# Kernel optimization log

Measured on AMD Instinct MI355X. Metric: run time of the kernel, lower is better.

## Reference

```python
import jax, jax.numpy as jnp
import numpy as np

NPOINT, K = 1024, 16
BN_EPS = 1e-5


def farthest_point_sample(xyz, npoint):
    # xyz: [B, N, 3]. Deterministic start at index 0 (torch version uses randint).
    B, N, _ = xyz.shape

    def step(carry, _):
        distance, farthest = carry
        centroid = jnp.take_along_axis(xyz, farthest[:, None, None], axis=1)  # [B,1,3]
        dist = jnp.sum((xyz - centroid) ** 2, axis=-1)  # [B,N]
        distance = jnp.minimum(distance, dist)
        nxt = jnp.argmax(distance, axis=-1)
        return (distance, nxt), farthest

    init = (jnp.full((B, N), 1e10, dtype=xyz.dtype), jnp.zeros((B,), dtype=jnp.int32))
    _, cents = jax.lax.scan(step, init, None, length=npoint)
    return jnp.transpose(cents)  # [B, npoint]


def knn_idx(k, xyz, new_xyz):
    # squared distances [B,S,N] via ||a||^2 + ||b||^2 - 2 a.b (avoids [B,S,N,3] blowup)
    d = (jnp.sum(new_xyz ** 2, -1)[:, :, None]
         + jnp.sum(xyz ** 2, -1)[:, None, :]
         - 2.0 * jnp.einsum('bsc,bnc->bsn', new_xyz, xyz))
    _, idx = jax.lax.top_k(-d, k)  # k smallest distances
    return idx


def gather_points(points, idx):
    # points: [B,N,C], idx: [B,...] -> [B,...,C]
    return jax.vmap(lambda p, i: p[i])(points, idx)


def bn_train(x, gamma, beta):
    # BatchNorm1d in train mode: batch statistics, biased variance
    m = jnp.mean(x, axis=0)
    v = jnp.var(x, axis=0)
    return gamma * (x - m) * jax.lax.rsqrt(v + BN_EPS) + beta


def setup_inputs() -> dict:
    key = jax.random.key(0)
    ks = jax.random.split(key, 16)
    B, N, CIN, COUT = 8, 4096, 64, 128
    cin3 = CIN + 3          # 67
    ec = int(cin3 * 2.0)    # 134 (expand_ratio=2, hidden_ch arg is unused by InvResMLP)
    s = 0.05
    return {
        'xyz': jax.random.normal(ks[0], (B, N, 3), jnp.float32),
        'pts': jax.random.normal(ks[1], (B, N, CIN), jnp.float32),
        'fc1_w': jax.random.normal(ks[2], (cin3, ec), jnp.float32) * s,
        'fc1_b': jnp.zeros((ec,), jnp.float32),
        'bn1_g': jnp.ones((ec,), jnp.float32),
        'bn1_b': jnp.zeros((ec,), jnp.float32),
        'fc2_w': jax.random.normal(ks[3], (ec, ec), jnp.float32) * s,
        'fc2_b': jnp.zeros((ec,), jnp.float32),
        'bn2_g': jnp.ones((ec,), jnp.float32),
        'bn2_b': jnp.zeros((ec,), jnp.float32),
        'fc3_w': jax.random.normal(ks[4], (ec, COUT), jnp.float32) * s,
        'fc3_b': jnp.zeros((COUT,), jnp.float32),
        'bn3_g': jnp.ones((COUT,), jnp.float32),
        'bn3_b': jnp.zeros((COUT,), jnp.float32),
        'sc_w': jax.random.normal(ks[5], (cin3, COUT), jnp.float32) * s,
        'sc_b': jnp.zeros((COUT,), jnp.float32),
        'scbn_g': jnp.ones((COUT,), jnp.float32),
        'scbn_b': jnp.zeros((COUT,), jnp.float32),
    }


def reference(xyz, pts, fc1_w, fc1_b, bn1_g, bn1_b, fc2_w, fc2_b, bn2_g, bn2_b,
              fc3_w, fc3_b, bn3_g, bn3_b, sc_w, sc_b, scbn_g, scbn_b):
    # --- local_group: FPS + kNN grouping ---
    cent = farthest_point_sample(xyz, NPOINT)          # [B,S]
    new_xyz = gather_points(xyz, cent)                 # [B,S,3]
    idx = knn_idx(K, xyz, new_xyz)                     # [B,S,K]
    grouped_xyz = gather_points(xyz, idx)              # [B,S,K,3]
    grouped_pts = gather_points(pts, idx)              # [B,S,K,C]
    grouped_xyz_norm = grouped_xyz - new_xyz[:, :, None, :]
    x = jnp.concatenate([grouped_xyz_norm, grouped_pts], axis=-1)  # [B,S,K,C+3]

    # --- InvResMLP (pointwise, train-mode BN, dropout as identity) ---
    B, S, Kk, C = x.shape
    x = x.reshape(B * S * Kk, C)
    sc = bn_train(x @ sc_w + sc_b, scbn_g, scbn_b)
    h = jax.nn.relu(bn_train(x @ fc1_w + fc1_b, bn1_g, bn1_b))
    h = jax.nn.relu(bn_train(h @ fc2_w + fc2_b, bn2_g, bn2_b))
    h = bn_train(h @ fc3_w + fc3_b, bn3_g, bn3_b)
    h = jax.nn.relu(h + sc)
    feats = h.reshape(B, S, Kk, -1)

    new_pts = jnp.max(feats, axis=2)                   # [B,S,out_ch]
    return new_xyz, new_pts
```

## Files before the change

kernel.cpp:

```cpp
#include <hip/hip_runtime.h>
#include <cstdint>
#include <cstddef>

typedef short short8 __attribute__((ext_vector_type(8)));
typedef float f32x4 __attribute__((ext_vector_type(4)));
typedef unsigned long long u64x2 __attribute__((ext_vector_type(2)));

#define B_   8
#define N_   4096
#define S_   1024
#define K_   16
#define M_   131072
#define CIN_ 64

__device__ inline float bf2f(unsigned short u) {
    unsigned int v = ((unsigned int)u) << 16;
    return __builtin_bit_cast(float, v);
}
__device__ inline unsigned short f2bf(float f) {
    unsigned int u = __builtin_bit_cast(unsigned int, f);
    unsigned int lsb = (u >> 16) & 1u;
    u += 0x7fffu + lsb;
    return (unsigned short)(u >> 16);
}

template<int CTRL>
__device__ inline unsigned long long dpp_max(unsigned long long k) {
    unsigned lo = (unsigned)k, hi = (unsigned)(k >> 32);
    unsigned olo = (unsigned)__builtin_amdgcn_update_dpp(0, (int)lo, CTRL, 0xF, 0xF, true);
    unsigned ohi = (unsigned)__builtin_amdgcn_update_dpp(0, (int)hi, CTRL, 0xF, 0xF, true);
    unsigned long long ok = ((unsigned long long)ohi << 32) | (unsigned long long)olo;
    return ok > k ? ok : k;
}

__global__ __launch_bounds__(256) void fps_aux_kernel(
    const float* __restrict__ xyz, float* __restrict__ outxyz,
    const float* __restrict__ fc1_w, const float* __restrict__ sc_w,
    const float* __restrict__ fc2_w, const float* __restrict__ fc3_w,
    unsigned short* __restrict__ WT1, unsigned short* __restrict__ WT2,
    unsigned short* __restrict__ WT3, float* __restrict__ sqn)
{
    __shared__ float px_s[N_], py_s[N_], pz_s[N_];
    __shared__ float sOut[S_ * 3];
    __shared__ unsigned long long sK[2][4];
    int t = threadIdx.x;

    if (blockIdx.x >= 8) {
        int aux = blockIdx.x - 8;
#pragma unroll
        for (int ch = 0; ch < 10; ch++) {
            int idx = (aux * 10 + ch) * 256 + t;
            if (idx < 13824) {
                int row = idx / 96, k = idx % 96;
                WT1[idx] = f2bf((k < 67 && row < 134) ? fc1_w[k * 134 + row] : 0.0f);
            } else if (idx < 26112) {
                int j = idx - 13824;
                int row = j / 96, k = j % 96;
                WT1[13824 + j] = f2bf((k < 67) ? sc_w[k * 128 + row] : 0.0f);
            } else if (idx < 49152) {
                int j = idx - 26112;
                int row = j / 160, k = j % 160;
                WT2[j] = f2bf((k < 134 && row < 134) ? fc2_w[k * 134 + row] : 0.0f);
            } else if (idx < 69632) {
                int j = idx - 49152;
                int row = j / 160, k = j % 160;
                WT3[j] = f2bf((k < 134) ? fc3_w[k * 128 + row] : 0.0f);
            } else {
                int i = idx - 69632;
                float x = xyz[i * 3 + 0], y = xyz[i * 3 + 1], z = xyz[i * 3 + 2];
                sqn[i] = __fadd_rn(__fadd_rn(__fmul_rn(x, x), __fmul_rn(y, y)),
                                   __fmul_rn(z, z));
            }
        }
        return;
    }

    int b = blockIdx.x;
    const float* xb = xyz + (size_t)b * N_ * 3;
    int w = t >> 6, l = t & 63;
    const int NP = 16;
    float px[NP], py[NP], pz[NP], dst[NP];
    int klo_[NP];
#pragma unroll
    for (int i = 0; i < NP; i++) {
        int p = i * 256 + t;
        px[i] = xb[p * 3 + 0];
        py[i] = xb[p * 3 + 1];
        pz[i] = xb[p * 3 + 2];
        dst[i] = 1e10f;
        klo_[i] = 4095 - p;
        px_s[p] = px[i]; py_s[p] = py[i]; pz_s[p] = pz[i];
        asm volatile("" : "+v"(px[i]), "+v"(py[i]), "+v"(pz[i]));
    }
    __syncthreads();
    float cx = px_s[0], cy = py_s[0], cz = pz_s[0];
    for (int s = 0; s < S_; s++) {
        if (t == 0) { sOut[s * 3 + 0] = cx; sOut[s * 3 + 1] = cy; sOut[s * 3 + 2] = cz; }
        if (s == S_ - 1) break;
        float bd = -1.0f; int bk = 0;
#pragma unroll
        for (int i = 0; i < NP; i++) {
            float dx = __fsub_rn(px[i], cx);
            float dy = __fsub_rn(py[i], cy);
            float dz = __fsub_rn(pz[i], cz);
            float d  = __fadd_rn(__fadd_rn(__fmul_rn(dx, dx), __fmul_rn(dy, dy)),
                                 __fmul_rn(dz, dz));
            float nd = fminf(dst[i], d);
            dst[i] = nd;
            if (nd > bd) { bd = nd; bk = klo_[i]; }
        }
        unsigned long long key =
            ((unsigned long long)__builtin_bit_cast(unsigned, bd) << 32) |
            (unsigned long long)(unsigned)bk;
        key = dpp_max<0xB1>(key);
        key = dpp_max<0x4E>(key);
        key = dpp_max<0x141>(key);
        key = dpp_max<0x140>(key);
        key = dpp_max<0x142>(key);
        key = dpp_max<0x143>(key);
        int par = s & 1;
        if (l == 63) sK[par][w] = key;
        __syncthreads();
        u64x2 kA = *(u64x2*)&sK[par][0];
        u64x2 kB = *(u64x2*)&sK[par][2];
        unsigned long long ka = kA[0] > kA[1] ? kA[0] : kA[1];
        unsigned long long kb = kB[0] > kB[1] ? kB[0] : kB[1];
        unsigned long long g  = ka > kb ? ka : kb;
        int p = 4095 - (int)(g & 0xFFFu);
        cx = px_s[p]; cy = py_s[p]; cz = pz_s[p];
    }
    __syncthreads();
    float* ob = outxyz + (size_t)b * S_ * 3;
    for (int i = t; i < S_ * 3; i += 256) ob[i] = sOut[i];
}

__global__ __launch_bounds__(256) void knn_build(const float* __restrict__ xyz,
                                                 const float* __restrict__ sqn,
                                                 const float* __restrict__ newxyz,
                                                 const float* __restrict__ pts,
                                                 unsigned short* __restrict__ X)
{
    __shared__ int sNbr[4][16];
    int w = threadIdx.x >> 6, l = threadIdx.x & 63;
    int q = blockIdx.x * 4 + w;
    int b = q >> 10;
    const float* xb = xyz + (size_t)b * N_ * 3;
    const float* sb = sqn + (size_t)b * N_;
    float qx = newxyz[(size_t)q * 3 + 0];
    float qy = newxyz[(size_t)q * 3 + 1];
    float qz = newxyz[(size_t)q * 3 + 2];
    float sa = __fadd_rn(__fadd_rn(__fmul_rn(qx, qx), __fmul_rn(qy, qy)), __fmul_rn(qz, qz));

    float d16[16]; int i16[16];
#pragma unroll
    for (int j = 0; j < 16; j++) { d16[j] = 3.0e38f; i16[j] = -1; }
    for (int i = 0; i < N_ / 64; i++) {
        int n = i * 64 + l;
        float bx = xb[n * 3 + 0], by = xb[n * 3 + 1], bz = xb[n * 3 + 2];
        float dot = __fmaf_rn(qz, bz, __fmaf_rn(qy, by, __fmul_rn(qx, bx)));
        float d = __fsub_rn(__fadd_rn(sa, sb[n]), __fmul_rn(2.0f, dot));
        if (d < d16[0]) {
            d16[0] = d; i16[0] = n;
#pragma unroll
            for (int j = 0; j < 15; j++) {
                if (d16[j] < d16[j + 1]) {
                    float td = d16[j]; d16[j] = d16[j + 1]; d16[j + 1] = td;
                    int   ti = i16[j]; i16[j] = i16[j + 1]; i16[j + 1] = ti;
                }
            }
        }
    }
#pragma unroll
    for (int r = 0; r < 16; r++) {
        float cd = d16[15]; int cn = i16[15];
#pragma unroll
        for (int off = 1; off < 64; off <<= 1) {
            float od = __shfl_xor(cd, off);
            int   on = __shfl_xor(cn, off);
            if (od < cd || (od == cd && on < cn)) { cd = od; cn = on; }
        }
        if (l == 0) sNbr[w][r] = cn;
        if (i16[15] == cn) {
#pragma unroll
            for (int j = 15; j >= 1; j--) { d16[j] = d16[j - 1]; i16[j] = i16[j - 1]; }
            d16[0] = 3.0e38f; i16[0] = -1;
        }
    }
    __syncthreads();
    int row = l >> 2, seg = l & 3;
    int n = sNbr[w][row];
    const float* pr = pts + ((size_t)b * N_ + n) * CIN_;
    const float* xr = xyz + ((size_t)b * N_ + n) * 3;
    float v[24];
#pragma unroll
    for (int e = 0; e < 24; e++) {
        int c = seg * 24 + e;
        float val;
        if (c == 0)      val = xr[0] - qx;
        else if (c == 1) val = xr[1] - qy;
        else if (c == 2) val = xr[2] - qz;
        else if (c < 67) val = pr[c - 3];
        else             val = 0.0f;
        v[e] = val;
    }
    short8 s0, s1, s2;
#pragma unroll
    for (int e = 0; e < 8; e++) {
        s0[e] = (short)f2bf(v[e]);
        s1[e] = (short)f2bf(v[8 + e]);
        s2[e] = (short)f2bf(v[16 + e]);
    }
    unsigned short* xp = X + ((size_t)q * 16 + row) * 96 + seg * 24;
    *(short8*)xp = s0;
    *(short8*)(xp + 8) = s1;
    *(short8*)(xp + 16) = s2;
}

template<int KPAD, int NF>
__global__ __launch_bounds__(256) void gemm_bn(
    const unsigned short* __restrict__ A, const unsigned short* __restrict__ Wt,
    unsigned short* __restrict__ Z1, int ld1, int n1real, float* sum1, float* sq1)
{
    __shared__ unsigned short sA[128 * KPAD];
    __shared__ float sSt[NF * 32];
    int t = threadIdx.x;
    int r0 = blockIdx.x * 128;
    for (int i = t; i < NF * 32; i += 256) sSt[i] = 0.0f;
    {
        const uint4* ga = (const uint4*)(A + (size_t)r0 * KPAD);
        uint4* la = (uint4*)sA;
        const int CNT = 128 * KPAD * 2 / 16;
        for (int i = t; i < CNT; i += 256) la[i] = ga[i];
    }
    __syncthreads();
    int w = t >> 6, l = t & 63, lhi = l >> 4, llo = l & 15;
    f32x4 acc[2][NF];
#pragma unroll
    for (int m = 0; m < 2; m++)
#pragma unroll
        for (int n = 0; n < NF; n++) acc[m][n] = (f32x4){0.f, 0.f, 0.f, 0.f};
#pragma unroll
    for (int ks = 0; ks < KPAD / 32; ks++) {
        short8 bfr[NF];
#pragma unroll
        for (int n = 0; n < NF; n++)
            bfr[n] = *(const short8*)(Wt + (size_t)(n * 16 + llo) * KPAD + ks * 32 + lhi * 8);
#pragma unroll
        for (int m = 0; m < 2; m++) {
            short8 afr = *(const short8*)(sA + (w * 32 + m * 16 + llo) * KPAD + ks * 32 + lhi * 8);
#pragma unroll
            for (int n = 0; n < NF; n++)
                acc[m][n] = __builtin_amdgcn_mfma_f32_16x16x32_bf16(afr, bfr[n], acc[m][n], 0, 0, 0);
        }
    }
#pragma unroll
    for (int n = 0; n < NF; n++) {
        int c = n * 16 + llo;
        float ss = 0.f, sq = 0.f;
#pragma unroll
        for (int m = 0; m < 2; m++) {
#pragma unroll
            for (int j = 0; j < 4; j++) {
                float v = acc[m][n][j];
                int row = r0 + w * 32 + m * 16 + lhi * 4 + j;
                Z1[(size_t)row * ld1 + c] = f2bf(v);
                ss += v; sq += v * v;
            }
        }
        ss += __shfl_xor(ss, 16); ss += __shfl_xor(ss, 32);
        sq += __shfl_xor(sq, 16); sq += __shfl_xor(sq, 32);
        if (l < 16) { atomicAdd(&sSt[c * 2], ss); atomicAdd(&sSt[c * 2 + 1], sq); }
    }
    __syncthreads();
    for (int c = t; c < NF * 16; c += 256) {
        if (c < n1real) {
            atomicAdd(&sum1[c], sSt[c * 2]);
            atomicAdd(&sq1[c], sSt[c * 2 + 1]);
        }
    }
}

__global__ __launch_bounds__(256) void norm_relu_v(const unsigned short* __restrict__ Z,
                                                   unsigned short* __restrict__ H,
                                                   const float* __restrict__ sum,
                                                   const float* __restrict__ sq,
                                                   const float* __restrict__ g,
                                                   const float* __restrict__ bb)
{
    __shared__ float sAC[272];
    int t = threadIdx.x;
    if (t < 136) {
        float a = 0.0f, c = 0.0f;
        if (t < 134) {
            const float inv = 1.0f / (float)M_;
            float m = sum[t] * inv;
            float var = sq[t] * inv - m * m;
            a = g[t] * rsqrtf(var + 1e-5f);
            c = bb[t] - a * m;
        }
        sAC[2 * t] = a; sAC[2 * t + 1] = c;
    }
    __syncthreads();
    int tid = blockIdx.x * 256 + t;
    int j = tid % 20;
    size_t r = (size_t)(tid / 20);
    int col0 = j * 8;
    short8 hv = {0, 0, 0, 0, 0, 0, 0, 0};
    if (col0 < 134) {
        short8 zv = *(const short8*)(Z + r * 144 + col0);
#pragma unroll
        for (int e = 0; e < 8; e++) {
            int col = col0 + e;
            float2 ac = *(float2*)&sAC[2 * col];
            float v = fmaxf(ac.x * bf2f((unsigned short)zv[e]) + ac.y, 0.0f);
            hv[e] = (col < 134) ? (short)f2bf(v) : (short)0;
        }
    }
    *(short8*)(H + r * 160 + col0) = hv;
}

__global__ __launch_bounds__(256) void final_kernel(
    const unsigned short* __restrict__ Z3, const unsigned short* __restrict__ ZSC,
    const float* __restrict__ sum3, const float* __restrict__ sq3,
    const float* __restrict__ g3, const float* __restrict__ b3,
    const float* __restrict__ sumsc, const float* __restrict__ sqsc,
    const float* __restrict__ gsc, const float* __restrict__ bsc,
    float* __restrict__ out)
{
    __shared__ float sF[512];
    int t = threadIdx.x;
    if (t < 128) {
        const float inv = 1.0f / (float)M_;
        float m3 = sum3[t] * inv, v3 = sq3[t] * inv - m3 * m3;
        float a3 = g3[t] * rsqrtf(v3 + 1e-5f), c3 = b3[t] - a3 * m3;
        float ms = sumsc[t] * inv, vs = sqsc[t] * inv - ms * ms;
        float as = gsc[t] * rsqrtf(vs + 1e-5f), cs = bsc[t] - as * ms;
        sF[t * 4 + 0] = a3; sF[t * 4 + 1] = c3; sF[t * 4 + 2] = as; sF[t * 4 + 3] = cs;
    }
    __syncthreads();
    int tid = blockIdx.x * 256 + t;
    int bs = tid >> 4, ch0 = (tid & 15) * 8;
    float A3[8], C3[8], AS[8], CS[8], mx[8];
#pragma unroll
    for (int e = 0; e < 8; e++) {
        f32x4 f = *(f32x4*)&sF[(ch0 + e) * 4];
        A3[e] = f[0]; C3[e] = f[1]; AS[e] = f[2]; CS[e] = f[3];
        mx[e] = 0.0f;
    }
    const unsigned short* z3p = Z3 + (size_t)bs * 16 * 128 + ch0;
    const unsigned short* zsp = ZSC + (size_t)bs * 16 * 128 + ch0;
#pragma unroll
    for (int k = 0; k < 16; k++) {
        short8 z3 = *(const short8*)(z3p + (size_t)k * 128);
        short8 zs = *(const short8*)(zsp + (size_t)k * 128);
#pragma unroll
        for (int e = 0; e < 8; e++) {
            float y = fmaxf(A3[e] * bf2f((unsigned short)z3[e]) + C3[e]
                            + AS[e] * bf2f((unsigned short)zs[e]) + CS[e], 0.0f);
            mx[e] = fmaxf(mx[e], y);
        }
    }
    float* op = out + 24576 + (size_t)bs * 128 + ch0;
#pragma unroll
    for (int e = 0; e < 8; e++) op[e] = mx[e];
}

#define WS_STATS 0
#define WS_WT1   8192
#define WS_WT2   61440
#define WS_WT3   108544
#define WS_SQN   149760
#define WS_X     281088
#define WS_Z     25447424
#define WS_ZSC   63196416
#define WS_H     96751104

extern "C" void kernel_launch(void* const* d_in, const int* in_sizes, int n_in,
                              void* d_out, int out_size, void* d_ws, size_t ws_size,
                              hipStream_t stream)
{
    const float* xyz    = (const float*)d_in[0];
    const float* pts    = (const float*)d_in[1];
    const float* fc1_w  = (const float*)d_in[2];
    const float* bn1_g  = (const float*)d_in[4];
    const float* bn1_b  = (const float*)d_in[5];
    const float* fc2_w  = (const float*)d_in[6];
    const float* bn2_g  = (const float*)d_in[8];
    const float* bn2_b  = (const float*)d_in[9];
    const float* fc3_w  = (const float*)d_in[10];
    const float* bn3_g  = (const float*)d_in[12];
    const float* bn3_b  = (const float*)d_in[13];
    const float* sc_w   = (const float*)d_in[14];
    const float* scbn_g = (const float*)d_in[16];
    const float* scbn_b = (const float*)d_in[17];

    char* ws = (char*)d_ws;
    float* st = (float*)(ws + WS_STATS);
    float* bn1_sum = st + 0,   *bn1_sq = st + 136;
    float* bnsc_sum = st + 272, *bnsc_sq = st + 400;
    float* bn2_sum = st + 528, *bn2_sq = st + 664;
    float* bn3_sum = st + 800, *bn3_sq = st + 928;

    unsigned short* WT1 = (unsigned short*)(ws + WS_WT1);
    unsigned short* WT2 = (unsigned short*)(ws + WS_WT2);
    unsigned short* WT3 = (unsigned short*)(ws + WS_WT3);
    float* SQN = (float*)(ws + WS_SQN);
    unsigned short* X   = (unsigned short*)(ws + WS_X);
    unsigned short* Z   = (unsigned short*)(ws + WS_Z);
    unsigned short* ZSC = (unsigned short*)(ws + WS_ZSC);
    unsigned short* H   = (unsigned short*)(ws + WS_H);
    float* out = (float*)d_out;

    hipMemsetAsync(ws + WS_STATS, 0, 1056 * 4, stream);

    fps_aux_kernel<<<48, 256, 0, stream>>>(xyz, out, fc1_w, sc_w, fc2_w, fc3_w,
                                           WT1, WT2, WT3, SQN);
    knn_build<<<2048, 256, 0, stream>>>(xyz, SQN, out, pts, X);

    gemm_bn<96, 9><<<1024, 256, 0, stream>>>(X, WT1, Z, 144, 134, bn1_sum, bn1_sq);
    gemm_bn<96, 8><<<1024, 256, 0, stream>>>(X, WT1 + 13824, ZSC, 128, 128, bnsc_sum, bnsc_sq);
    norm_relu_v<<<10240, 256, 0, stream>>>(Z, H, bn1_sum, bn1_sq, bn1_g, bn1_b);

    gemm_bn<160, 9><<<1024, 256, 0, stream>>>(H, WT2, Z, 144, 134, bn2_sum, bn2_sq);
    norm_relu_v<<<10240, 256, 0, stream>>>(Z, H, bn2_sum, bn2_sq, bn2_g, bn2_b);

    gemm_bn<160, 8><<<1024, 256, 0, stream>>>(H, WT3, Z, 128, 128, bn3_sum, bn3_sq);

    final_kernel<<<512, 256, 0, stream>>>(Z, ZSC, bn3_sum, bn3_sq, bn3_g, bn3_b,
                                          bnsc_sum, bnsc_sq, scbn_g, scbn_b, out);
}
```

Baseline: 1.037 ms.

## Fuse BN-normalize+ReLU into next GEMM prologue and merge first-layer GEMMs

Removes the two standalone norm_relu kernels by applying batch-norm scale/shift and ReLU while staging the previous layer's pre-activation into shared memory inside the next GEMM. The two first-layer GEMMs (fc1 and shortcut) are merged into one 2048-block launch. GEMM outputs are now staged through padded shared memory and written with coalesced 16-byte stores, and A tiles use a padded stride to reduce bank conflicts. FPS drops the per-point index register array, computing the index inline. This cuts two full passes over the intermediate activation and two launches, at the cost of extra prologue work and more LDS per block.

Measured after the change: 972.6 us. 1.07x faster.

```diff
diff --git a/kernel.cpp b/kernel.cpp
--- a/kernel.cpp
+++ b/kernel.cpp
@@ -42,7 +42,7 @@
 {
     __shared__ float px_s[N_], py_s[N_], pz_s[N_];
     __shared__ float sOut[S_ * 3];
-    __shared__ unsigned long long sK[2][4];
+    __shared__ __attribute__((aligned(16))) unsigned long long sK[2][4];
     int t = threadIdx.x;
 
     if (blockIdx.x >= 8) {
@@ -80,7 +80,6 @@
     int w = t >> 6, l = t & 63;
     const int NP = 16;
     float px[NP], py[NP], pz[NP], dst[NP];
-    int klo_[NP];
 #pragma unroll
     for (int i = 0; i < NP; i++) {
         int p = i * 256 + t;
@@ -88,7 +87,6 @@
         py[i] = xb[p * 3 + 1];
         pz[i] = xb[p * 3 + 2];
         dst[i] = 1e10f;
-        klo_[i] = 4095 - p;
         px_s[p] = px[i]; py_s[p] = py[i]; pz_s[p] = pz[i];
         asm volatile("" : "+v"(px[i]), "+v"(py[i]), "+v"(pz[i]));
     }
@@ -97,7 +95,7 @@
     for (int s = 0; s < S_; s++) {
         if (t == 0) { sOut[s * 3 + 0] = cx; sOut[s * 3 + 1] = cy; sOut[s * 3 + 2] = cz; }
         if (s == S_ - 1) break;
-        float bd = -1.0f; int bk = 0;
+        float bd = -1.0f; int bp = 0;
 #pragma unroll
         for (int i = 0; i < NP; i++) {
             float dx = __fsub_rn(px[i], cx);
@@ -107,11 +105,11 @@
                                  __fmul_rn(dz, dz));
             float nd = fminf(dst[i], d);
             dst[i] = nd;
-            if (nd > bd) { bd = nd; bk = klo_[i]; }
+            if (nd > bd) { bd = nd; bp = i * 256 + t; }
         }
         unsigned long long key =
             ((unsigned long long)__builtin_bit_cast(unsigned, bd) << 32) |
-            (unsigned long long)(unsigned)bk;
+            (unsigned long long)(unsigned)(4095 - bp);
         key = dpp_max<0xB1>(key);
         key = dpp_max<0x4E>(key);
         key = dpp_max<0x141>(key);
@@ -216,21 +214,53 @@
     *(short8*)(xp + 16) = s2;
 }
 
-template<int KPAD, int NF>
-__global__ __launch_bounds__(256) void gemm_bn(
+template<int KPAD, int NF, bool BNST>
+__device__ __forceinline__ void gemm_core(
     const unsigned short* __restrict__ A, const unsigned short* __restrict__ Wt,
-    unsigned short* __restrict__ Z1, int ld1, int n1real, float* sum1, float* sq1)
-{
-    __shared__ unsigned short sA[128 * KPAD];
-    __shared__ float sSt[NF * 32];
-    int t = threadIdx.x;
-    int r0 = blockIdx.x * 128;
+    unsigned short* __restrict__ Zo, float* __restrict__ sum, float* __restrict__ sq,
+    int nreal, const float* __restrict__ ps, const float* __restrict__ pq,
+    const float* __restrict__ pg, const float* __restrict__ pb,
+    int r0, unsigned short* sBuf, float* sSt, float* sAC, int t)
+{
+    constexpr int AST = KPAD + 8;
     for (int i = t; i < NF * 32; i += 256) sSt[i] = 0.0f;
-    {
-        const uint4* ga = (const uint4*)(A + (size_t)r0 * KPAD);
-        uint4* la = (uint4*)sA;
-        const int CNT = 128 * KPAD * 2 / 16;
-        for (int i = t; i < CNT; i += 256) la[i] = ga[i];
+    if (BNST) {
+        if (t < 160) {
+            float a = 0.f, c = 0.f;
+            if (t < 134) {
+                const float inv = 1.0f / (float)M_;
+                float m = ps[t] * inv;
+                float var = pq[t] * inv - m * m;
+                a = pg[t] * rsqrtf(var + 1e-5f);
+                c = pb[t] - a * m;
+            }
+            sAC[2 * t] = a; sAC[2 * t + 1] = c;
+        }
+        __syncthreads();
+#pragma unroll
+        for (int c8 = 0; c8 < 10; c8++) {
+            int chunk = c8 * 256 + t;
+            int row = chunk / 20, col0 = (chunk % 20) * 8;
+            short8 hv = {0, 0, 0, 0, 0, 0, 0, 0};
+            if (col0 < 144) {
+                short8 zv = *(const short8*)(A + (size_t)(r0 + row) * 144 + col0);
+#pragma unroll
+                for (int e = 0; e < 8; e++) {
+                    float2 ac = *(float2*)&sAC[2 * (col0 + e)];
+                    float v = fmaxf(ac.x * bf2f((unsigned short)zv[e]) + ac.y, 0.0f);
+                    hv[e] = (short)f2bf(v);
+                }
+            }
+            *(short8*)(sBuf + row * AST + col0) = hv;
+        }
+    } else {
+#pragma unroll
+        for (int c8 = 0; c8 < (128 * KPAD / 8) / 256; c8++) {
+            int chunk = c8 * 256 + t;
+            int row = chunk / (KPAD / 8), col0 = (chunk % (KPAD / 8)) * 8;
+            *(short8*)(sBuf + row * AST + col0) =
+                *(const short8*)(A + (size_t)(r0 + row) * KPAD + col0);
+        }
     }
     __syncthreads();
     int w = t >> 6, l = t & 63, lhi = l >> 4, llo = l & 15;
@@ -247,76 +277,88 @@
             bfr[n] = *(const short8*)(Wt + (size_t)(n * 16 + llo) * KPAD + ks * 32 + lhi * 8);
 #pragma unroll
         for (int m = 0; m < 2; m++) {
-            short8 afr = *(const short8*)(sA + (w * 32 + m * 16 + llo) * KPAD + ks * 32 + lhi * 8);
+            short8 afr = *(const short8*)(sBuf + (w * 32 + m * 16 + llo) * AST + ks * 32 + lhi * 8);
 #pragma unroll
             for (int n = 0; n < NF; n++)
                 acc[m][n] = __builtin_amdgcn_mfma_f32_16x16x32_bf16(afr, bfr[n], acc[m][n], 0, 0, 0);
         }
     }
+    __syncthreads();
+    constexpr int OST = NF * 16 + 8;
 #pragma unroll
     for (int n = 0; n < NF; n++) {
         int c = n * 16 + llo;
-        float ss = 0.f, sq = 0.f;
+        float ss = 0.f, sqv = 0.f;
 #pragma unroll
         for (int m = 0; m < 2; m++) {
 #pragma unroll
             for (int j = 0; j < 4; j++) {
                 float v = acc[m][n][j];
-                int row = r0 + w * 32 + m * 16 + lhi * 4 + j;
-                Z1[(size_t)row * ld1 + c] = f2bf(v);
-                ss += v; sq += v * v;
+                int row = w * 32 + m * 16 + lhi * 4 + j;
+                sBuf[row * OST + c] = f2bf(v);
+                ss += v; sqv += v * v;
             }
         }
         ss += __shfl_xor(ss, 16); ss += __shfl_xor(ss, 32);
-        sq += __shfl_xor(sq, 16); sq += __shfl_xor(sq, 32);
-        if (l < 16) { atomicAdd(&sSt[c * 2], ss); atomicAdd(&sSt[c * 2 + 1], sq); }
-    }
-    __syncthreads();
+        sqv += __shfl_xor(sqv, 16); sqv += __shfl_xor(sqv, 32);
+        if (l < 16) { atomicAdd(&sSt[c * 2], ss); atomicAdd(&sSt[c * 2 + 1], sqv); }
+    }
+    __syncthreads();
+#pragma unroll
+    for (int c8 = 0; c8 < NF; c8++) {
+        int chunk = c8 * 256 + t;
+        int row = chunk / (NF * 2), cc = chunk % (NF * 2);
+        *(short8*)(Zo + (size_t)(r0 + row) * (NF * 16) + cc * 8) =
+            *(const short8*)(sBuf + row * OST + cc * 8);
+    }
     for (int c = t; c < NF * 16; c += 256) {
-        if (c < n1real) {
-            atomicAdd(&sum1[c], sSt[c * 2]);
-            atomicAdd(&sq1[c], sSt[c * 2 + 1]);
-        }
-    }
-}
-
-__global__ __launch_bounds__(256) void norm_relu_v(const unsigned short* __restrict__ Z,
-                                                   unsigned short* __restrict__ H,
-                                                   const float* __restrict__ sum,
-                                                   const float* __restrict__ sq,
-                                                   const float* __restrict__ g,
-                                                   const float* __restrict__ bb)
-{
-    __shared__ float sAC[272];
+        if (c < nreal) {
+            atomicAdd(&sum[c], sSt[c * 2]);
+            atomicAdd(&sq[c], sSt[c * 2 + 1]);
+        }
+    }
+}
+
+__global__ __launch_bounds__(256) void gemm1_fused(
+    const unsigned short* __restrict__ X, const unsigned short* __restrict__ WT1,
+    unsigned short* __restrict__ Z1, unsigned short* __restrict__ ZSC,
+    float* s1, float* q1, float* ssc, float* qsc)
+{
+    __shared__ unsigned short sBuf[21504];
+    __shared__ float sSt[288];
     int t = threadIdx.x;
-    if (t < 136) {
-        float a = 0.0f, c = 0.0f;
-        if (t < 134) {
-            const float inv = 1.0f / (float)M_;
-            float m = sum[t] * inv;
-            float var = sq[t] * inv - m * m;
-            a = g[t] * rsqrtf(var + 1e-5f);
-            c = bb[t] - a * m;
-        }
-        sAC[2 * t] = a; sAC[2 * t + 1] = c;
-    }
-    __syncthreads();
-    int tid = blockIdx.x * 256 + t;
-    int j = tid % 20;
-    size_t r = (size_t)(tid / 20);
-    int col0 = j * 8;
-    short8 hv = {0, 0, 0, 0, 0, 0, 0, 0};
-    if (col0 < 134) {
-        short8 zv = *(const short8*)(Z + r * 144 + col0);
-#pragma unroll
-        for (int e = 0; e < 8; e++) {
-            int col = col0 + e;
-            float2 ac = *(float2*)&sAC[2 * col];
-            float v = fmaxf(ac.x * bf2f((unsigned short)zv[e]) + ac.y, 0.0f);
-            hv[e] = (col < 134) ? (short)f2bf(v) : (short)0;
-        }
-    }
-    *(short8*)(H + r * 160 + col0) = hv;
+    if (blockIdx.x < 1024)
+        gemm_core<96, 9, false>(X, WT1, Z1, s1, q1, 134,
+                                nullptr, nullptr, nullptr, nullptr,
+                                blockIdx.x * 128, sBuf, sSt, nullptr, t);
+    else
+        gemm_core<96, 8, false>(X, WT1 + 13824, ZSC, ssc, qsc, 128,
+                                nullptr, nullptr, nullptr, nullptr,
+                                (blockIdx.x - 1024) * 128, sBuf, sSt, nullptr, t);
+}
+
+__global__ __launch_bounds__(256) void gemm_l2(
+    const unsigned short* __restrict__ Zin, const unsigned short* __restrict__ WT,
+    unsigned short* __restrict__ Zout, float* sum, float* sq,
+    const float* ps, const float* pq, const float* pg, const float* pb)
+{
+    __shared__ unsigned short sBuf[21504];
+    __shared__ float sSt[288];
+    __shared__ float sAC[320];
+    gemm_core<160, 9, true>(Zin, WT, Zout, sum, sq, 134, ps, pq, pg, pb,
+                            blockIdx.x * 128, sBuf, sSt, sAC, threadIdx.x);
+}
+
+__global__ __launch_bounds__(256) void gemm_l3(
+    const unsigned short* __restrict__ Zin, const unsigned short* __restrict__ WT,
+    unsigned short* __restrict__ Zout, float* sum, float* sq,
+    const float* ps, const float* pq, const float* pg, const float* pb)
+{
+    __shared__ unsigned short sBuf[21504];
+    __shared__ float sSt[288];
+    __shared__ float sAC[320];
+    gemm_core<160, 8, true>(Zin, WT, Zout, sum, sq, 128, ps, pq, pg, pb,
+                            blockIdx.x * 128, sBuf, sSt, sAC, threadIdx.x);
 }
 
 __global__ __launch_bounds__(256) void final_kernel(
@@ -371,9 +413,9 @@
 #define WS_WT3   108544
 #define WS_SQN   149760
 #define WS_X     281088
-#define WS_Z     25447424
+#define WS_Z1    25447424
 #define WS_ZSC   63196416
-#define WS_H     96751104
+#define WS_Z2    96751104
 
 extern "C" void kernel_launch(void* const* d_in, const int* in_sizes, int n_in,
                               void* d_out, int out_size, void* d_ws, size_t ws_size,
@@ -396,19 +438,20 @@
 
     char* ws = (char*)d_ws;
     float* st = (float*)(ws + WS_STATS);
-    float* bn1_sum = st + 0,   *bn1_sq = st + 136;
+    float* bn1_sum = st + 0,    *bn1_sq = st + 136;
     float* bnsc_sum = st + 272, *bnsc_sq = st + 400;
-    float* bn2_sum = st + 528, *bn2_sq = st + 664;
-    float* bn3_sum = st + 800, *bn3_sq = st + 928;
+    float* bn2_sum = st + 528,  *bn2_sq = st + 664;
+    float* bn3_sum = st + 800,  *bn3_sq = st + 928;
 
     unsigned short* WT1 = (unsigned short*)(ws + WS_WT1);
     unsigned short* WT2 = (unsigned short*)(ws + WS_WT2);
     unsigned short* WT3 = (unsigned short*)(ws + WS_WT3);
     float* SQN = (float*)(ws + WS_SQN);
     unsigned short* X   = (unsigned short*)(ws + WS_X);
-    unsigned short* Z   = (unsigned short*)(ws + WS_Z);
+    unsigned short* Z1  = (unsigned short*)(ws + WS_Z1);
     unsigned short* ZSC = (unsigned short*)(ws + WS_ZSC);
-    unsigned short* H   = (unsigned short*)(ws + WS_H);
+    unsigned short* Z2  = (unsigned short*)(ws + WS_Z2);
+    unsigned short* Z3  = Z1;
     float* out = (float*)d_out;
 
     hipMemsetAsync(ws + WS_STATS, 0, 1056 * 4, stream);
@@ -417,15 +460,13 @@
                                            WT1, WT2, WT3, SQN);
     knn_build<<<2048, 256, 0, stream>>>(xyz, SQN, out, pts, X);
 
-    gemm_bn<96, 9><<<1024, 256, 0, stream>>>(X, WT1, Z, 144, 134, bn1_sum, bn1_sq);
-    gemm_bn<96, 8><<<1024, 256, 0, stream>>>(X, WT1 + 13824, ZSC, 128, 128, bnsc_sum, bnsc_sq);
-    norm_relu_v<<<10240, 256, 0, stream>>>(Z, H, bn1_sum, bn1_sq, bn1_g, bn1_b);
-
-    gemm_bn<160, 9><<<1024, 256, 0, stream>>>(H, WT2, Z, 144, 134, bn2_sum, bn2_sq);
-    norm_relu_v<<<10240, 256, 0, stream>>>(Z, H, bn2_sum, bn2_sq, bn2_g, bn2_b);
-
-    gemm_bn<160, 8><<<1024, 256, 0, stream>>>(H, WT3, Z, 128, 128, bn3_sum, bn3_sq);
-
-    final_kernel<<<512, 256, 0, stream>>>(Z, ZSC, bn3_sum, bn3_sq, bn3_g, bn3_b,
+    gemm1_fused<<<2048, 256, 0, stream>>>(X, WT1, Z1, ZSC,
+                                          bn1_sum, bn1_sq, bnsc_sum, bnsc_sq);
+    gemm_l2<<<1024, 256, 0, stream>>>(Z1, WT2, Z2, bn2_sum, bn2_sq,
+                                      bn1_sum, bn1_sq, bn1_g, bn1_b);
+    gemm_l3<<<1024, 256, 0, stream>>>(Z2, WT3, Z3, bn3_sum, bn3_sq,
+                                      bn2_sum, bn2_sq, bn2_g, bn2_b);
+
+    final_kernel<<<512, 256, 0, stream>>>(Z3, ZSC, bn3_sum, bn3_sq, bn3_g, bn3_b,
                                           bnsc_sum, bnsc_sq, scbn_g, scbn_b, out);
 }
```
